# Kernel tuning notes

Hardware: AMD Instinct MI355X
Metric: run time of the kernel (lower is better)

Reference implementation:

```python
import jax, jax.numpy as jnp
import numpy as np

B, N, D = 8, 256, 128
LN_EPS = 1e-5


def setup_inputs() -> dict:
    key = jax.random.key(0)
    ks = jax.random.split(key, 12)
    s = 0.02
    return {
        "node_features": jax.random.normal(ks[0], (B, N, D), dtype=jnp.float32),
        "adjacency": jax.random.uniform(ks[1], (B, N, N), dtype=jnp.float32),
        "msg_w1": jax.random.normal(ks[2], (2 * D, D), dtype=jnp.float32) * s,
        "msg_b1": jnp.zeros((D,), jnp.float32),
        "msg_w2": jax.random.normal(ks[3], (D, D), dtype=jnp.float32) * s,
        "msg_b2": jnp.zeros((D,), jnp.float32),
        "upd_w1": jax.random.normal(ks[4], (2 * D, D), dtype=jnp.float32) * s,
        "upd_b1": jnp.zeros((D,), jnp.float32),
        "upd_w2": jax.random.normal(ks[5], (D, D), dtype=jnp.float32) * s,
        "upd_b2": jnp.zeros((D,), jnp.float32),
        "ln_g": jnp.ones((D,), jnp.float32),
        "ln_b": jnp.zeros((D,), jnp.float32),
    }


def reference(node_features, adjacency, msg_w1, msg_b1, msg_w2, msg_b2,
              upd_w1, upd_b1, upd_w2, upd_b2, ln_g, ln_b):
    d = node_features.shape[-1]
    n = node_features.shape[1]
    # Split the concat-then-matmul: cat(x_i, x_j) @ W1 == x_i @ W1[:d] + x_j @ W1[d:]
    hi = node_features @ msg_w1[:d]          # [B,N,D] (receiver i contribution)
    hj = node_features @ msg_w1[d:]          # [B,N,D] (sender j contribution)
    h = jax.nn.relu(hi[:, :, None, :] + hj[:, None, :, :] + msg_b1)  # [B,N,N,D]
    # Edge weights with the i==j pairs excluded (loop skips self-edges)
    a = adjacency * (1.0 - jnp.eye(n, dtype=adjacency.dtype))        # [B,N,N]
    # sum_j (h @ W2 + b2) * a_ij  ==  (sum_j h * a_ij) @ W2 + b2 * sum_j a_ij
    s = jnp.einsum('bijd,bij->bid', h, a)    # [B,N,D]
    agg = s @ msg_w2 + msg_b2 * jnp.sum(a, axis=-1, keepdims=True)   # [B,N,D]
    u = jnp.concatenate([node_features, agg], axis=-1)               # [B,N,2D]
    upd = jax.nn.relu(u @ upd_w1 + upd_b1) @ upd_w2 + upd_b2         # [B,N,D]
    res = node_features + upd
    mu = jnp.mean(res, axis=-1, keepdims=True)
    var = jnp.var(res, axis=-1, keepdims=True)
    return (res - mu) / jnp.sqrt(var + LN_EPS) * ln_g + ln_b
```

## Files before the change

kernel.cpp:

```cpp
#include <hip/hip_runtime.h>

#define BB 8
#define NN 256
#define DD 128
#define LN_EPS 1e-5f

__global__ __launch_bounds__(512) void k_proj(const float* __restrict__ x,
                                              const float* __restrict__ w1,
                                              const float* __restrict__ b1,
                                              float* __restrict__ hi,
                                              float* __restrict__ hjb) {
    __shared__ float xs[8][DD];
    __shared__ float part_a[4][8][DD];
    __shared__ float part_b[4][8][DD];
    const int bid  = blockIdx.x;
    const int row0 = (bid & 7) * NN + (bid >> 3) * 8;
    const int tid  = threadIdx.x;
    #pragma unroll
    for (int t = tid; t < 8 * DD; t += 512)
        xs[t >> 7][t & 127] = x[row0 * DD + t];
    __syncthreads();

    const int dp = tid & 127;
    const int kg = tid >> 7;
    const int kb = kg * 32;

    float acc_a[8] = {}, acc_b[8] = {};
    #pragma unroll
    for (int k4 = 0; k4 < 8; ++k4) {
        const int k0 = kb + k4 * 4;
        float wa[4], wb[4];
        #pragma unroll
        for (int q = 0; q < 4; ++q) {
            wa[q] = w1[(k0 + q) * DD + dp];
            wb[q] = w1[(DD + k0 + q) * DD + dp];
        }
        #pragma unroll
        for (int r = 0; r < 8; ++r) {
            const float4 xv = *(const float4*)&xs[r][k0];
            acc_a[r] = fmaf(xv.x, wa[0], acc_a[r]);
            acc_a[r] = fmaf(xv.y, wa[1], acc_a[r]);
            acc_a[r] = fmaf(xv.z, wa[2], acc_a[r]);
            acc_a[r] = fmaf(xv.w, wa[3], acc_a[r]);
            acc_b[r] = fmaf(xv.x, wb[0], acc_b[r]);
            acc_b[r] = fmaf(xv.y, wb[1], acc_b[r]);
            acc_b[r] = fmaf(xv.z, wb[2], acc_b[r]);
            acc_b[r] = fmaf(xv.w, wb[3], acc_b[r]);
        }
    }
    #pragma unroll
    for (int r = 0; r < 8; ++r) {
        part_a[kg][r][dp] = acc_a[r];
        part_b[kg][r][dp] = acc_b[r];
    }
    __syncthreads();
    #pragma unroll
    for (int m = 0; m < 2; ++m) {
        int idx = tid + m * 512;
        int r = idx >> 7, d = idx & 127;
        float sa = part_a[0][r][d] + part_a[1][r][d] + part_a[2][r][d] + part_a[3][r][d];
        float sb = part_b[0][r][d] + part_b[1][r][d] + part_b[2][r][d] + part_b[3][r][d];
        hi [(row0 + r) * DD + d] = sa;
        hjb[(row0 + r) * DD + d] = sb + b1[d];
    }
}

__global__ __launch_bounds__(512) void k_fused(const float* __restrict__ adj,
                                               const float* __restrict__ x,
                                               const float* __restrict__ hi,
                                               const float* __restrict__ hjb,
                                               const float* __restrict__ w2,
                                               const float* __restrict__ b2,
                                               const float* __restrict__ w3,
                                               const float* __restrict__ b3,
                                               const float* __restrict__ w4,
                                               const float* __restrict__ b4,
                                               const float* __restrict__ g,
                                               const float* __restrict__ bet,
                                               float* __restrict__ out) {
    __shared__ float smem[13320];
    float* const a_t    = smem + 8192;
    float* const xs     = smem + 10240;
    float* const ssp    = smem + 11264;
    float* const aggs   = smem + 12288;
    float* const u1s    = smem + 8192;
    float* const resS   = smem + 9216;
    float* const part   = smem;
    float* const asum_s = smem + 13312;

    const int bid = blockIdx.x;
    const int b   = bid & 7;
    const int i0  = (bid >> 3) * 8;
    const int tid = threadIdx.x;

    #pragma unroll
    for (int t = 0; t < 4; ++t) {
        int idx = tid + t * 512;
        int il = idx >> 8, j = idx & 255;
        int i_g = i0 + il;
        float av = adj[((size_t)b * NN + i_g) * NN + j];
        a_t[il * 256 + j] = (j == i_g) ? 0.f : av;
    }
    #pragma unroll
    for (int t = 0; t < 2; ++t) {
        int idx = tid + t * 512;
        xs[idx] = x[((size_t)b * NN + i0) * DD + idx];
    }
    __syncthreads();

    {
        int w = tid >> 6, l = tid & 63;
        float s = a_t[w * 256 + l] + a_t[w * 256 + l + 64]
                + a_t[w * 256 + l + 128] + a_t[w * 256 + l + 192];
        #pragma unroll
        for (int m = 32; m; m >>= 1) s += __shfl_xor(s, m);
        if (l == 0) asum_s[w] = s;
    }

    const int dq  = tid & 31;
    const int rg  = tid >> 5;
    const int row = rg & 7;
    const int jh  = rg >> 3;
    const float4 hi4 = *(const float4*)&hi[((size_t)b * NN + i0 + row) * DD + dq * 4];
    float4 acc = {0.f, 0.f, 0.f, 0.f};

    for (int jt = 0; jt < 4; ++jt) {
        __syncthreads();
        const float4* src = (const float4*)(hjb + ((size_t)b * NN + jt * 64) * DD);
        float4* dst = (float4*)smem;
        #pragma unroll
        for (int t = 0; t < 4; ++t) dst[tid + t * 512] = src[tid + t * 512];
        __syncthreads();
        const int jb = jh * 32;
        #pragma unroll 8
        for (int jj = 0; jj < 32; ++jj) {
            const int jl = jb + jj;
            const float4 hv = *(const float4*)&smem[jl * 128 + dq * 4];
            const float a = a_t[row * 256 + jt * 64 + jl];
            acc.x = fmaf(fmaxf(hi4.x + hv.x, 0.f), a, acc.x);
            acc.y = fmaf(fmaxf(hi4.y + hv.y, 0.f), a, acc.y);
            acc.z = fmaf(fmaxf(hi4.z + hv.z, 0.f), a, acc.z);
            acc.w = fmaf(fmaxf(hi4.w + hv.w, 0.f), a, acc.w);
        }
    }
    __syncthreads();
    *(float4*)&ssp[rg * 128 + dq * 4] = acc;
    __syncthreads();
    #pragma unroll
    for (int t = 0; t < 2; ++t) {
        int idx = tid + t * 512;
        int r = idx >> 7, d = idx & 127;
        ssp[r * 128 + d] += ssp[(r + 8) * 128 + d];
    }
    __syncthreads();

    const int dp = tid & 63;
    const int kg = tid >> 6;
    const int kb = kg * 16;

    {
        float wv0[16], wv1[16];
        #pragma unroll
        for (int k = 0; k < 16; ++k) {
            wv0[k] = w2[(kb + k) * DD + dp];
            wv1[k] = w2[(kb + k) * DD + dp + 64];
        }
        #pragma unroll
        for (int r = 0; r < 8; ++r) {
            float a0 = 0.f, a1 = 0.f;
            #pragma unroll
            for (int q = 0; q < 4; ++q) {
                const float4 sv = *(const float4*)&ssp[r * 128 + kb + q * 4];
                a0 = fmaf(sv.x, wv0[q*4+0], a0); a1 = fmaf(sv.x, wv1[q*4+0], a1);
                a0 = fmaf(sv.y, wv0[q*4+1], a0); a1 = fmaf(sv.y, wv1[q*4+1], a1);
                a0 = fmaf(sv.z, wv0[q*4+2], a0); a1 = fmaf(sv.z, wv1[q*4+2], a1);
                a0 = fmaf(sv.w, wv0[q*4+3], a0); a1 = fmaf(sv.w, wv1[q*4+3], a1);
            }
            part[kg * 1024 + r * 128 + dp]      = a0;
            part[kg * 1024 + r * 128 + dp + 64] = a1;
        }
    }
    __syncthreads();
    #pragma unroll
    for (int m = 0; m < 2; ++m) {
        int idx = tid + m * 512;
        int r = idx >> 7, d = idx & 127;
        float s = part[r * 128 + d];
        #pragma unroll
        for (int w = 1; w < 8; ++w) s += part[w * 1024 + r * 128 + d];
        aggs[r * 128 + d] = s + b2[d] * asum_s[r];
    }
    __syncthreads();

    {
        float wa0[16], wa1[16], wb0[16], wb1[16];
        #pragma unroll
        for (int k = 0; k < 16; ++k) {
            wa0[k] = w3[(kb + k) * DD + dp];
            wa1[k] = w3[(kb + k) * DD + dp + 64];
            wb0[k] = w3[(DD + kb + k) * DD + dp];
            wb1[k] = w3[(DD + kb + k) * DD + dp + 64];
        }
        #pragma unroll
        for (int r = 0; r < 8; ++r) {
            float a0 = 0.f, a1 = 0.f;
            #pragma unroll
            for (int q = 0; q < 4; ++q) {
                const float4 xv = *(const float4*)&xs[r * 128 + kb + q * 4];
                const float4 av = *(const float4*)&aggs[r * 128 + kb + q * 4];
                a0 = fmaf(xv.x, wa0[q*4+0], a0); a1 = fmaf(xv.x, wa1[q*4+0], a1);
                a0 = fmaf(xv.y, wa0[q*4+1], a0); a1 = fmaf(xv.y, wa1[q*4+1], a1);
                a0 = fmaf(xv.z, wa0[q*4+2], a0); a1 = fmaf(xv.z, wa1[q*4+2], a1);
                a0 = fmaf(xv.w, wa0[q*4+3], a0); a1 = fmaf(xv.w, wa1[q*4+3], a1);
                a0 = fmaf(av.x, wb0[q*4+0], a0); a1 = fmaf(av.x, wb1[q*4+0], a1);
                a0 = fmaf(av.y, wb0[q*4+1], a0); a1 = fmaf(av.y, wb1[q*4+1], a1);
                a0 = fmaf(av.z, wb0[q*4+2], a0); a1 = fmaf(av.z, wb1[q*4+2], a1);
                a0 = fmaf(av.w, wb0[q*4+3], a0); a1 = fmaf(av.w, wb1[q*4+3], a1);
            }
            part[kg * 1024 + r * 128 + dp]      = a0;
            part[kg * 1024 + r * 128 + dp + 64] = a1;
        }
    }
    __syncthreads();
    #pragma unroll
    for (int m = 0; m < 2; ++m) {
        int idx = tid + m * 512;
        int r = idx >> 7, d = idx & 127;
        float s = part[r * 128 + d];
        #pragma unroll
        for (int w = 1; w < 8; ++w) s += part[w * 1024 + r * 128 + d];
        u1s[r * 128 + d] = fmaxf(s + b3[d], 0.f);
    }
    __syncthreads();

    {
        float wv0[16], wv1[16];
        #pragma unroll
        for (int k = 0; k < 16; ++k) {
            wv0[k] = w4[(kb + k) * DD + dp];
            wv1[k] = w4[(kb + k) * DD + dp + 64];
        }
        #pragma unroll
        for (int r = 0; r < 8; ++r) {
            float a0 = 0.f, a1 = 0.f;
            #pragma unroll
            for (int q = 0; q < 4; ++q) {
                const float4 uv = *(const float4*)&u1s[r * 128 + kb + q * 4];
                a0 = fmaf(uv.x, wv0[q*4+0], a0); a1 = fmaf(uv.x, wv1[q*4+0], a1);
                a0 = fmaf(uv.y, wv0[q*4+1], a0); a1 = fmaf(uv.y, wv1[q*4+1], a1);
                a0 = fmaf(uv.z, wv0[q*4+2], a0); a1 = fmaf(uv.z, wv1[q*4+2], a1);
                a0 = fmaf(uv.w, wv0[q*4+3], a0); a1 = fmaf(uv.w, wv1[q*4+3], a1);
            }
            part[kg * 1024 + r * 128 + dp]      = a0;
            part[kg * 1024 + r * 128 + dp + 64] = a1;
        }
    }
    __syncthreads();
    #pragma unroll
    for (int m = 0; m < 2; ++m) {
        int idx = tid + m * 512;
        int r = idx >> 7, d = idx & 127;
        float s = part[r * 128 + d];
        #pragma unroll
        for (int w = 1; w < 8; ++w) s += part[w * 1024 + r * 128 + d];
        resS[r * 128 + d] = xs[r * 128 + d] + s + b4[d];
    }
    __syncthreads();

    {
        const int r = tid >> 6, l = tid & 63;
        const float2 v = *(const float2*)&resS[r * 128 + l * 2];
        float s1 = v.x + v.y;
        float s2 = v.x * v.x + v.y * v.y;
        #pragma unroll
        for (int m = 32; m; m >>= 1) {
            s1 += __shfl_xor(s1, m);
            s2 += __shfl_xor(s2, m);
        }
        const float mu = s1 * (1.f / DD);
        const float rs = rsqrtf(s2 * (1.f / DD) - mu * mu + LN_EPS);
        const int d = l * 2;
        const float2 gv = *(const float2*)&g[d];
        const float2 bv = *(const float2*)&bet[d];
        float2 o;
        o.x = (v.x - mu) * rs * gv.x + bv.x;
        o.y = (v.y - mu) * rs * gv.y + bv.y;
        *(float2*)&out[((size_t)b * NN + i0 + r) * DD + d] = o;
    }
}

extern "C" void kernel_launch(void* const* d_in, const int* in_sizes, int n_in,
                              void* d_out, int out_size, void* d_ws, size_t ws_size,
                              hipStream_t stream) {
    (void)in_sizes; (void)n_in; (void)out_size; (void)ws_size;
    const float* x      = (const float*)d_in[0];
    const float* adj    = (const float*)d_in[1];
    const float* msg_w1 = (const float*)d_in[2];
    const float* msg_b1 = (const float*)d_in[3];
    const float* msg_w2 = (const float*)d_in[4];
    const float* msg_b2 = (const float*)d_in[5];
    const float* upd_w1 = (const float*)d_in[6];
    const float* upd_b1 = (const float*)d_in[7];
    const float* upd_w2 = (const float*)d_in[8];
    const float* upd_b2 = (const float*)d_in[9];
    const float* ln_g   = (const float*)d_in[10];
    const float* ln_b   = (const float*)d_in[11];
    float* out = (float*)d_out;

    const size_t BND = (size_t)BB * NN * DD;
    float* ws  = (float*)d_ws;
    float* hi  = ws;
    float* hjb = ws + BND;

    k_proj<<<dim3(256), dim3(512), 0, stream>>>(x, msg_w1, msg_b1, hi, hjb);
    k_fused<<<dim3(256), dim3(512), 0, stream>>>(adj, x, hi, hjb,
                                                 msg_w2, msg_b2,
                                                 upd_w1, upd_b1, upd_w2, upd_b2,
                                                 ln_g, ln_b, out);
}
```

Before: 27.17 us.

## Register-block edge aggregation over four receiver rows with transposed adjacency tile

The edge-aggregation loop now has each thread accumulate four receiver rows instead of one. Each hj vector loaded from shared memory is reused four times, and the adjacency tile is stored transposed so four row weights come in as one float4. Work is split across j by wave, so partial sums from 8 waves are reduced through shared memory instead of 2. The adjacency row sums are now computed with wave shuffles during the load. This cuts LDS reads per FMA, at the cost of more registers and a larger reduction step.

Measured after the change: 27.61 us. No clear change (+1.6%).

```diff
diff --git a/kernel.cpp b/kernel.cpp
--- a/kernel.cpp
+++ b/kernel.cpp
@@ -78,28 +78,38 @@
                                                const float* __restrict__ g,
                                                const float* __restrict__ bet,
                                                float* __restrict__ out) {
-    __shared__ float smem[13320];
-    float* const a_t    = smem + 8192;
+    __shared__ float smem[13352];
+    float* const hjs    = smem;
+    float* const partP  = smem;
+    float* const partT  = smem;
+    float* const a_tt   = smem + 8192;
+    float* const u1s    = smem + 8192;
+    float* const resS   = smem + 9216;
     float* const xs     = smem + 10240;
     float* const ssp    = smem + 11264;
     float* const aggs   = smem + 12288;
-    float* const u1s    = smem + 8192;
-    float* const resS   = smem + 9216;
-    float* const part   = smem;
-    float* const asum_s = smem + 13312;
-
-    const int bid = blockIdx.x;
-    const int b   = bid & 7;
-    const int i0  = (bid >> 3) * 8;
-    const int tid = threadIdx.x;
+    float* const asub   = smem + 13312;
+    float* const asum_s = smem + 13344;
+
+    const int bid  = blockIdx.x;
+    const int b    = bid & 7;
+    const int i0   = (bid >> 3) * 8;
+    const int tid  = threadIdx.x;
+    const int lane = tid & 63;
+    const int wv   = tid >> 6;
 
     #pragma unroll
     for (int t = 0; t < 4; ++t) {
         int idx = tid + t * 512;
         int il = idx >> 8, j = idx & 255;
-        int i_g = i0 + il;
-        float av = adj[((size_t)b * NN + i_g) * NN + j];
-        a_t[il * 256 + j] = (j == i_g) ? 0.f : av;
+        int ig = i0 + il;
+        float av = adj[((size_t)b * NN + ig) * NN + j];
+        av = (j == ig) ? 0.f : av;
+        a_tt[j * 8 + il] = av;
+        float s = av;
+        #pragma unroll
+        for (int m = 32; m; m >>= 1) s += __shfl_xor(s, m);
+        if (lane == 0) asub[il * 4 + ((idx >> 6) & 3)] = s;
     }
     #pragma unroll
     for (int t = 0; t < 2; ++t) {
@@ -108,49 +118,55 @@
     }
     __syncthreads();
 
-    {
-        int w = tid >> 6, l = tid & 63;
-        float s = a_t[w * 256 + l] + a_t[w * 256 + l + 64]
-                + a_t[w * 256 + l + 128] + a_t[w * 256 + l + 192];
-        #pragma unroll
-        for (int m = 32; m; m >>= 1) s += __shfl_xor(s, m);
-        if (l == 0) asum_s[w] = s;
-    }
-
-    const int dq  = tid & 31;
-    const int rg  = tid >> 5;
-    const int row = rg & 7;
-    const int jh  = rg >> 3;
-    const float4 hi4 = *(const float4*)&hi[((size_t)b * NN + i0 + row) * DD + dq * 4];
-    float4 acc = {0.f, 0.f, 0.f, 0.f};
+    const int dq = lane & 31;
+    const int rh = lane >> 5;
+    float4 hi4[4];
+    #pragma unroll
+    for (int rr = 0; rr < 4; ++rr)
+        hi4[rr] = *(const float4*)&hi[((size_t)b * NN + i0 + rh * 4 + rr) * DD + dq * 4];
+    float4 acc[4] = {{0,0,0,0},{0,0,0,0},{0,0,0,0},{0,0,0,0}};
 
     for (int jt = 0; jt < 4; ++jt) {
         __syncthreads();
         const float4* src = (const float4*)(hjb + ((size_t)b * NN + jt * 64) * DD);
-        float4* dst = (float4*)smem;
+        float4* dst = (float4*)hjs;
         #pragma unroll
         for (int t = 0; t < 4; ++t) dst[tid + t * 512] = src[tid + t * 512];
         __syncthreads();
-        const int jb = jh * 32;
-        #pragma unroll 8
-        for (int jj = 0; jj < 32; ++jj) {
+        const int jb = wv * 8;
+        #pragma unroll
+        for (int jj = 0; jj < 8; ++jj) {
             const int jl = jb + jj;
-            const float4 hv = *(const float4*)&smem[jl * 128 + dq * 4];
-            const float a = a_t[row * 256 + jt * 64 + jl];
-            acc.x = fmaf(fmaxf(hi4.x + hv.x, 0.f), a, acc.x);
-            acc.y = fmaf(fmaxf(hi4.y + hv.y, 0.f), a, acc.y);
-            acc.z = fmaf(fmaxf(hi4.z + hv.z, 0.f), a, acc.z);
-            acc.w = fmaf(fmaxf(hi4.w + hv.w, 0.f), a, acc.w);
-        }
-    }
-    __syncthreads();
-    *(float4*)&ssp[rg * 128 + dq * 4] = acc;
-    __syncthreads();
+            const float4 hv = *(const float4*)&hjs[jl * DD + dq * 4];
+            const float4 a4 = *(const float4*)&a_tt[(jt * 64 + jl) * 8 + rh * 4];
+            const float aa[4] = {a4.x, a4.y, a4.z, a4.w};
+            #pragma unroll
+            for (int rr = 0; rr < 4; ++rr) {
+                acc[rr].x = fmaf(fmaxf(hi4[rr].x + hv.x, 0.f), aa[rr], acc[rr].x);
+                acc[rr].y = fmaf(fmaxf(hi4[rr].y + hv.y, 0.f), aa[rr], acc[rr].y);
+                acc[rr].z = fmaf(fmaxf(hi4[rr].z + hv.z, 0.f), aa[rr], acc[rr].z);
+                acc[rr].w = fmaf(fmaxf(hi4[rr].w + hv.w, 0.f), aa[rr], acc[rr].w);
+            }
+        }
+    }
+    __syncthreads();
+    {
+        float* pp = partP + wv * 1024 + rh * 4 * DD;
+        #pragma unroll
+        for (int rr = 0; rr < 4; ++rr)
+            *(float4*)&pp[rr * DD + dq * 4] = acc[rr];
+    }
+    __syncthreads();
+    if (tid < 8)
+        asum_s[tid] = asub[tid * 4] + asub[tid * 4 + 1]
+                    + asub[tid * 4 + 2] + asub[tid * 4 + 3];
     #pragma unroll
     for (int t = 0; t < 2; ++t) {
         int idx = tid + t * 512;
-        int r = idx >> 7, d = idx & 127;
-        ssp[r * 128 + d] += ssp[(r + 8) * 128 + d];
+        float s = 0.f;
+        #pragma unroll
+        for (int w = 0; w < 8; ++w) s += partP[w * 1024 + idx];
+        ssp[idx] = s;
     }
     __syncthreads();
 
@@ -176,8 +192,8 @@
                 a0 = fmaf(sv.z, wv0[q*4+2], a0); a1 = fmaf(sv.z, wv1[q*4+2], a1);
                 a0 = fmaf(sv.w, wv0[q*4+3], a0); a1 = fmaf(sv.w, wv1[q*4+3], a1);
             }
-            part[kg * 1024 + r * 128 + dp]      = a0;
-            part[kg * 1024 + r * 128 + dp + 64] = a1;
+            partT[kg * 1024 + r * 128 + dp]      = a0;
+            partT[kg * 1024 + r * 128 + dp + 64] = a1;
         }
     }
     __syncthreads();
@@ -185,10 +201,10 @@
     for (int m = 0; m < 2; ++m) {
         int idx = tid + m * 512;
         int r = idx >> 7, d = idx & 127;
-        float s = part[r * 128 + d];
-        #pragma unroll
-        for (int w = 1; w < 8; ++w) s += part[w * 1024 + r * 128 + d];
-        aggs[r * 128 + d] = s + b2[d] * asum_s[r];
+        float s = partT[idx];
+        #pragma unroll
+        for (int w = 1; w < 8; ++w) s += partT[w * 1024 + idx];
+        aggs[idx] = s + b2[d] * asum_s[r];
     }
     __syncthreads();
 
@@ -217,8 +233,8 @@
                 a0 = fmaf(av.z, wb0[q*4+2], a0); a1 = fmaf(av.z, wb1[q*4+2], a1);
                 a0 = fmaf(av.w, wb0[q*4+3], a0); a1 = fmaf(av.w, wb1[q*4+3], a1);
             }
-            part[kg * 1024 + r * 128 + dp]      = a0;
-            part[kg * 1024 + r * 128 + dp + 64] = a1;
+            partT[kg * 1024 + r * 128 + dp]      = a0;
+            partT[kg * 1024 + r * 128 + dp + 64] = a1;
         }
     }
     __syncthreads();
@@ -226,10 +242,10 @@
     for (int m = 0; m < 2; ++m) {
         int idx = tid + m * 512;
         int r = idx >> 7, d = idx & 127;
-        float s = part[r * 128 + d];
-        #pragma unroll
-        for (int w = 1; w < 8; ++w) s += part[w * 1024 + r * 128 + d];
-        u1s[r * 128 + d] = fmaxf(s + b3[d], 0.f);
+        float s = partT[idx];
+        #pragma unroll
+        for (int w = 1; w < 8; ++w) s += partT[w * 1024 + idx];
+        u1s[idx] = fmaxf(s + b3[d], 0.f);
     }
     __syncthreads();
 
@@ -251,8 +267,8 @@
                 a0 = fmaf(uv.z, wv0[q*4+2], a0); a1 = fmaf(uv.z, wv1[q*4+2], a1);
                 a0 = fmaf(uv.w, wv0[q*4+3], a0); a1 = fmaf(uv.w, wv1[q*4+3], a1);
             }
-            part[kg * 1024 + r * 128 + dp]      = a0;
-            part[kg * 1024 + r * 128 + dp + 64] = a1;
+            partT[kg * 1024 + r * 128 + dp]      = a0;
+            partT[kg * 1024 + r * 128 + dp + 64] = a1;
         }
     }
     __syncthreads();
@@ -260,10 +276,10 @@
     for (int m = 0; m < 2; ++m) {
         int idx = tid + m * 512;
         int r = idx >> 7, d = idx & 127;
-        float s = part[r * 128 + d];
-        #pragma unroll
-        for (int w = 1; w < 8; ++w) s += part[w * 1024 + r * 128 + d];
-        resS[r * 128 + d] = xs[r * 128 + d] + s + b4[d];
+        float s = partT[idx];
+        #pragma unroll
+        for (int w = 1; w < 8; ++w) s += partT[w * 1024 + idx];
+        resS[idx] = xs[idx] + s + b4[d];
     }
     __syncthreads();
 
```

## Fuse projection into main kernel with per-batch atomic grid barrier

Applied to the files above, without the earlier changes.

Merges the projection kernel into the fused kernel, so only one kernel is launched. Each block computes its own hi rows into shared memory and publishes its hjb rows to global memory. A per-batch atomic counter then waits until all 32 blocks of that batch have finished before hjb is read. This removes a launch and the global round trip for hi, and the adjacency load overlaps the barrier wait. It relies on all 256 blocks being resident at once, and on the counter reset logic being correct across repeated calls.

After: 100.2 us. 269% more time.

```diff
diff --git a/kernel.cpp b/kernel.cpp
--- a/kernel.cpp
+++ b/kernel.cpp
@@ -5,108 +5,124 @@
 #define DD 128
 #define LN_EPS 1e-5f
 
-__global__ __launch_bounds__(512) void k_proj(const float* __restrict__ x,
+__device__ int g_cnt[BB];
+__device__ int g_done[BB];
+
+__global__ __launch_bounds__(512) void kf_all(const float* __restrict__ adj,
+                                              const float* __restrict__ x,
                                               const float* __restrict__ w1,
                                               const float* __restrict__ b1,
-                                              float* __restrict__ hi,
-                                              float* __restrict__ hjb) {
-    __shared__ float xs[8][DD];
-    __shared__ float part_a[4][8][DD];
-    __shared__ float part_b[4][8][DD];
-    const int bid  = blockIdx.x;
-    const int row0 = (bid & 7) * NN + (bid >> 3) * 8;
-    const int tid  = threadIdx.x;
-    #pragma unroll
-    for (int t = tid; t < 8 * DD; t += 512)
-        xs[t >> 7][t & 127] = x[row0 * DD + t];
-    __syncthreads();
-
-    const int dp = tid & 127;
-    const int kg = tid >> 7;
-    const int kb = kg * 32;
-
-    float acc_a[8] = {}, acc_b[8] = {};
-    #pragma unroll
-    for (int k4 = 0; k4 < 8; ++k4) {
-        const int k0 = kb + k4 * 4;
-        float wa[4], wb[4];
-        #pragma unroll
-        for (int q = 0; q < 4; ++q) {
-            wa[q] = w1[(k0 + q) * DD + dp];
-            wb[q] = w1[(DD + k0 + q) * DD + dp];
-        }
-        #pragma unroll
-        for (int r = 0; r < 8; ++r) {
-            const float4 xv = *(const float4*)&xs[r][k0];
-            acc_a[r] = fmaf(xv.x, wa[0], acc_a[r]);
-            acc_a[r] = fmaf(xv.y, wa[1], acc_a[r]);
-            acc_a[r] = fmaf(xv.z, wa[2], acc_a[r]);
-            acc_a[r] = fmaf(xv.w, wa[3], acc_a[r]);
-            acc_b[r] = fmaf(xv.x, wb[0], acc_b[r]);
-            acc_b[r] = fmaf(xv.y, wb[1], acc_b[r]);
-            acc_b[r] = fmaf(xv.z, wb[2], acc_b[r]);
-            acc_b[r] = fmaf(xv.w, wb[3], acc_b[r]);
-        }
-    }
-    #pragma unroll
-    for (int r = 0; r < 8; ++r) {
-        part_a[kg][r][dp] = acc_a[r];
-        part_b[kg][r][dp] = acc_b[r];
-    }
-    __syncthreads();
-    #pragma unroll
-    for (int m = 0; m < 2; ++m) {
-        int idx = tid + m * 512;
-        int r = idx >> 7, d = idx & 127;
-        float sa = part_a[0][r][d] + part_a[1][r][d] + part_a[2][r][d] + part_a[3][r][d];
-        float sb = part_b[0][r][d] + part_b[1][r][d] + part_b[2][r][d] + part_b[3][r][d];
-        hi [(row0 + r) * DD + d] = sa;
-        hjb[(row0 + r) * DD + d] = sb + b1[d];
-    }
-}
-
-__global__ __launch_bounds__(512) void k_fused(const float* __restrict__ adj,
-                                               const float* __restrict__ x,
-                                               const float* __restrict__ hi,
-                                               const float* __restrict__ hjb,
-                                               const float* __restrict__ w2,
-                                               const float* __restrict__ b2,
-                                               const float* __restrict__ w3,
-                                               const float* __restrict__ b3,
-                                               const float* __restrict__ w4,
-                                               const float* __restrict__ b4,
-                                               const float* __restrict__ g,
-                                               const float* __restrict__ bet,
-                                               float* __restrict__ out) {
-    __shared__ float smem[13320];
+                                              const float* __restrict__ w2,
+                                              const float* __restrict__ b2,
+                                              const float* __restrict__ w3,
+                                              const float* __restrict__ b3,
+                                              const float* __restrict__ w4,
+                                              const float* __restrict__ b4,
+                                              const float* __restrict__ g,
+                                              const float* __restrict__ bet,
+                                              float* __restrict__ hjb,
+                                              float* __restrict__ out) {
+    __shared__ float smem[14344];
+    float* const part   = smem;
     float* const a_t    = smem + 8192;
+    float* const u1s    = smem + 8192;
+    float* const resS   = smem + 9216;
     float* const xs     = smem + 10240;
     float* const ssp    = smem + 11264;
     float* const aggs   = smem + 12288;
-    float* const u1s    = smem + 8192;
-    float* const resS   = smem + 9216;
-    float* const part   = smem;
     float* const asum_s = smem + 13312;
-
-    const int bid = blockIdx.x;
-    const int b   = bid & 7;
-    const int i0  = (bid >> 3) * 8;
-    const int tid = threadIdx.x;
+    float* const his    = smem + 13320;
+
+    const int bid   = blockIdx.x;
+    const int b     = bid & 7;
+    const int i0    = (bid >> 3) * 8;
+    const int row0g = b * NN + i0;
+    const int tid   = threadIdx.x;
+
+    #pragma unroll
+    for (int t = 0; t < 2; ++t) {
+        int idx = tid + t * 512;
+        xs[idx] = x[row0g * DD + idx];
+    }
+    __syncthreads();
+
+    {
+        const int dp = tid & 127;
+        const int kg = tid >> 7;
+        const int kb = kg * 32;
+        float acc_a[8] = {}, acc_b[8] = {};
+        #pragma unroll
+        for (int k4 = 0; k4 < 8; ++k4) {
+            const int k0 = kb + k4 * 4;
+            float wa[4], wb[4];
+            #pragma unroll
+            for (int q = 0; q < 4; ++q) {
+                wa[q] = w1[(k0 + q) * DD + dp];
+                wb[q] = w1[(DD + k0 + q) * DD + dp];
+            }
+            #pragma unroll
+            for (int r = 0; r < 8; ++r) {
+                const float4 xv = *(const float4*)&xs[r * DD + k0];
+                acc_a[r] = fmaf(xv.x, wa[0], acc_a[r]);
+                acc_a[r] = fmaf(xv.y, wa[1], acc_a[r]);
+                acc_a[r] = fmaf(xv.z, wa[2], acc_a[r]);
+                acc_a[r] = fmaf(xv.w, wa[3], acc_a[r]);
+                acc_b[r] = fmaf(xv.x, wb[0], acc_b[r]);
+                acc_b[r] = fmaf(xv.y, wb[1], acc_b[r]);
+                acc_b[r] = fmaf(xv.z, wb[2], acc_b[r]);
+                acc_b[r] = fmaf(xv.w, wb[3], acc_b[r]);
+            }
+        }
+        #pragma unroll
+        for (int r = 0; r < 8; ++r) {
+            part[kg * 1024 + r * DD + dp]        = acc_a[r];
+            part[4096 + kg * 1024 + r * DD + dp] = acc_b[r];
+        }
+    }
+    __syncthreads();
+    #pragma unroll
+    for (int m = 0; m < 2; ++m) {
+        int idx = tid + m * 512;
+        int r = idx >> 7, d = idx & 127;
+        float sa = 0.f, sb = 0.f;
+        #pragma unroll
+        for (int w = 0; w < 4; ++w) {
+            sa += part[w * 1024 + r * DD + d];
+            sb += part[4096 + w * 1024 + r * DD + d];
+        }
+        his[r * DD + d] = sa;
+        hjb[(size_t)(row0g + r) * DD + d] = sb + b1[d];
+    }
+    __threadfence();
+    __syncthreads();
+    if (tid == 0)
+        __hip_atomic_fetch_add(&g_cnt[b], 1, __ATOMIC_RELEASE,
+                               __HIP_MEMORY_SCOPE_AGENT);
 
     #pragma unroll
     for (int t = 0; t < 4; ++t) {
         int idx = tid + t * 512;
         int il = idx >> 8, j = idx & 255;
-        int i_g = i0 + il;
-        float av = adj[((size_t)b * NN + i_g) * NN + j];
-        a_t[il * 256 + j] = (j == i_g) ? 0.f : av;
-    }
-    #pragma unroll
-    for (int t = 0; t < 2; ++t) {
-        int idx = tid + t * 512;
-        xs[idx] = x[((size_t)b * NN + i0) * DD + idx];
-    }
-    __syncthreads();
+        int ig = i0 + il;
+        float av = adj[((size_t)b * NN + ig) * NN + j];
+        a_t[il * 256 + j] = (j == ig) ? 0.f : av;
+    }
+
+    if (tid == 0) {
+        while (__hip_atomic_load(&g_cnt[b], __ATOMIC_ACQUIRE,
+                                 __HIP_MEMORY_SCOPE_AGENT) < 32)
+            __builtin_amdgcn_s_sleep(2);
+        int od = __hip_atomic_fetch_add(&g_done[b], 1, __ATOMIC_RELAXED,
+                                        __HIP_MEMORY_SCOPE_AGENT);
+        if (od == 31) {
+            __hip_atomic_store(&g_cnt[b], 0, __ATOMIC_RELAXED,
+                               __HIP_MEMORY_SCOPE_AGENT);
+            __hip_atomic_store(&g_done[b], 0, __ATOMIC_RELAXED,
+                               __HIP_MEMORY_SCOPE_AGENT);
+        }
+    }
+    __syncthreads();
+    __threadfence();
 
     {
         int w = tid >> 6, l = tid & 63;
@@ -121,7 +137,7 @@
     const int rg  = tid >> 5;
     const int row = rg & 7;
     const int jh  = rg >> 3;
-    const float4 hi4 = *(const float4*)&hi[((size_t)b * NN + i0 + row) * DD + dq * 4];
+    const float4 hi4 = *(const float4*)&his[row * DD + dq * 4];
     float4 acc = {0.f, 0.f, 0.f, 0.f};
 
     for (int jt = 0; jt < 4; ++jt) {
@@ -185,10 +201,10 @@
     for (int m = 0; m < 2; ++m) {
         int idx = tid + m * 512;
         int r = idx >> 7, d = idx & 127;
-        float s = part[r * 128 + d];
-        #pragma unroll
-        for (int w = 1; w < 8; ++w) s += part[w * 1024 + r * 128 + d];
-        aggs[r * 128 + d] = s + b2[d] * asum_s[r];
+        float s = part[idx];
+        #pragma unroll
+        for (int w = 1; w < 8; ++w) s += part[w * 1024 + idx];
+        aggs[idx] = s + b2[d] * asum_s[r];
     }
     __syncthreads();
 
@@ -226,10 +242,10 @@
     for (int m = 0; m < 2; ++m) {
         int idx = tid + m * 512;
         int r = idx >> 7, d = idx & 127;
-        float s = part[r * 128 + d];
-        #pragma unroll
-        for (int w = 1; w < 8; ++w) s += part[w * 1024 + r * 128 + d];
-        u1s[r * 128 + d] = fmaxf(s + b3[d], 0.f);
+        float s = part[idx];
+        #pragma unroll
+        for (int w = 1; w < 8; ++w) s += part[w * 1024 + idx];
+        u1s[idx] = fmaxf(s + b3[d], 0.f);
     }
     __syncthreads();
 
@@ -260,10 +276,10 @@
     for (int m = 0; m < 2; ++m) {
         int idx = tid + m * 512;
         int r = idx >> 7, d = idx & 127;
-        float s = part[r * 128 + d];
-        #pragma unroll
-        for (int w = 1; w < 8; ++w) s += part[w * 1024 + r * 128 + d];
-        resS[r * 128 + d] = xs[r * 128 + d] + s + b4[d];
+        float s = part[idx];
+        #pragma unroll
+        for (int w = 1; w < 8; ++w) s += part[w * 1024 + idx];
+        resS[idx] = xs[idx] + s + b4[d];
     }
     __syncthreads();
 
@@ -307,14 +323,10 @@
     const float* ln_b   = (const float*)d_in[11];
     float* out = (float*)d_out;
 
-    const size_t BND = (size_t)BB * NN * DD;
-    float* ws  = (float*)d_ws;
-    float* hi  = ws;
-    float* hjb = ws + BND;
-
-    k_proj<<<dim3(256), dim3(512), 0, stream>>>(x, msg_w1, msg_b1, hi, hjb);
-    k_fused<<<dim3(256), dim3(512), 0, stream>>>(adj, x, hi, hjb,
-                                                 msg_w2, msg_b2,
-                                                 upd_w1, upd_b1, upd_w2, upd_b2,
-                                                 ln_g, ln_b, out);
+    float* hjb = (float*)d_ws;
+
+    kf_all<<<dim3(256), dim3(512), 0, stream>>>(adj, x, msg_w1, msg_b1,
+                                                msg_w2, msg_b2,
+                                                upd_w1, upd_b1, upd_w2, upd_b2,
+                                                ln_g, ln_b, hjb, out);
 }
```
